# Performance work log

Hardware: AMD Instinct MI355X
Metric: run time of the kernel (lower is better)

The kernel has to match this reference:

```python
import jax, jax.numpy as jnp
import numpy as np

# MXInt config (mirrors q_config in init_kwargs)
A_MW, A_EW = 8, 4   # matmul input A mantissa/exponent widths
B_MW, B_EW = 8, 4   # matmul input B
O_MW, O_EW = 8, 4   # matmul output
SM_MW, SM_EW = 8, 4 # softmax output


def _dequant(m, e, mw):
    # m: [..., S, D] integer-valued mantissas; e: [..., S] shared row exponent
    # value = m * 2^(e - mw + 1)
    return m * jnp.exp2(e.astype(m.dtype)[..., None] - (mw - 1))


def _quant(x, mw, ew):
    # MXInt block quantization with exponent shared over the last dim.
    amax = jnp.max(jnp.abs(x), axis=-1)
    e = jnp.floor(jnp.log2(jnp.maximum(amax, jnp.exp2(jnp.float32(-126)))))
    e = jnp.clip(e, -(2 ** (ew - 1)), 2 ** (ew - 1) - 1)
    m = jnp.round(x * jnp.exp2(-(e[..., None] - (mw - 1))))
    m = jnp.clip(m, -(2 ** (mw - 1)), 2 ** (mw - 1) - 1)
    return m, e


def setup_inputs() -> dict:
    key = jax.random.key(0)
    ks = jax.random.split(key, 6)
    B, S, D = 256, 512, 64
    mquery = jax.random.randint(ks[0], (B, S, D), 0, 128).astype(jnp.float32)
    mkey = jax.random.randint(ks[1], (B, S, D), 0, 128).astype(jnp.float32)
    mvalue = jax.random.randint(ks[2], (B, S, D), 0, 128).astype(jnp.float32)
    equery = jax.random.randint(ks[3], (B, S), 0, 6, dtype=jnp.int32)
    ekey = jax.random.randint(ks[4], (B, S), 0, 6, dtype=jnp.int32)
    evalue = jax.random.randint(ks[5], (B, S), 0, 6, dtype=jnp.int32)
    return {"mquery": mquery, "equery": equery, "mkey": mkey,
            "ekey": ekey, "mvalue": mvalue, "evalue": evalue}


def reference(mquery, equery, mkey, ekey, mvalue, evalue):
    # QK^T in dequantized domain, then requantize output to MXInt (per-row exp)
    q = _dequant(mquery, equery, A_MW)            # [B,S,D]
    k = _dequant(mkey, ekey, B_MW)                # [B,S,D]
    scores = jnp.einsum('bsd,btd->bst', q, k)     # [B,S,S]
    m_s, _e_s = _quant(scores, O_MW, O_EW)
    # Note: the torch module calls the softmax on the score MANTISSAS only
    # (the score exponent is dropped), then requantizes the probabilities.
    probs = jax.nn.softmax(m_s, axis=-1)
    m_p, e_p = _quant(probs, SM_MW, SM_EW)
    # AV matmul: dequant probs with A widths, values with B widths
    p = _dequant(m_p, e_p, A_MW)                  # [B,S,S]
    v = _dequant(mvalue, evalue, B_MW)            # [B,S,D]
    ctx = jnp.einsum('bst,btd->bsd', p, v)        # [B,S,D]
    m_c, e_c = _quant(ctx, O_MW, O_EW)
    # final dequant exactly as the module: m * 2^(e - OUT_MAN_WIDTH + 1)
    return m_c * jnp.exp2(e_c[..., None] - O_MW + 1)
```

## Files before the change

### kernel.cpp

```cpp
#include <hip/hip_runtime.h>
#include <math.h>

#define S_LEN 512
#define D_DIM 64

typedef __attribute__((ext_vector_type(8))) short bf16x8;
typedef __attribute__((ext_vector_type(4))) float f32x4;
typedef __attribute__((ext_vector_type(4))) unsigned int u32x4;
typedef unsigned int u32;
typedef unsigned long long u64;

__device__ __forceinline__ float pow2i(int e) {
    return __int_as_float((e + 127) << 23);
}
__device__ __forceinline__ u32 pack_bf2(float lo, float hi) {
    return __builtin_amdgcn_perm(__float_as_uint(hi), __float_as_uint(lo), 0x07060302u);
}

extern "C" __global__ void __launch_bounds__(512, 2)
mxattn(const float* __restrict__ gmq, const int* __restrict__ geq,
       const float* __restrict__ gmk, const int* __restrict__ gek,
       const float* __restrict__ gmv, const int* __restrict__ gev,
       float* __restrict__ gout)
{
    __shared__ __attribute__((aligned(16))) short Ktile[32768];
    __shared__ __attribute__((aligned(16))) short Vtile[32768];
    __shared__ __attribute__((aligned(16))) char Pex[8 * 2 * 64 * 16];
    __shared__ __attribute__((aligned(16))) float evtab[S_LEN];

    const int b    = blockIdx.x;
    const int tid  = threadIdx.x;
    const int lane = tid & 63;
    const int wave = tid >> 6;
    const int l15  = lane & 15;
    const int lg   = lane >> 4;

    const float* mqb = gmq + (size_t)b * (S_LEN * D_DIM);
    const float* mkb = gmk + (size_t)b * (S_LEN * D_DIM);
    const float* mvb = gmv + (size_t)b * (S_LEN * D_DIM);
    const int* eqb = geq + b * S_LEN;
    const int* ekb = gek + b * S_LEN;
    const int* evb = gev + b * S_LEN;

    char* kb = (char*)Ktile;
    char* vb = (char*)Vtile;

    evtab[tid] = pow2i(evb[tid] - 7);
    #pragma unroll
    for (int i = 0; i < 4; ++i) {
        int tt = wave * 4 + i;
        int t = tt * 16 + l15;
        float ks = pow2i(ekb[t] - 7);
        const float* kp = mkb + t * 64 + lg * 8;
        f32x4 a0 = *(const f32x4*)(kp);
        f32x4 a1 = *(const f32x4*)(kp + 4);
        f32x4 a2 = *(const f32x4*)(kp + 32);
        f32x4 a3 = *(const f32x4*)(kp + 36);
        u32x4 w0 = { pack_bf2(a0[0] * ks, a0[1] * ks), pack_bf2(a0[2] * ks, a0[3] * ks),
                     pack_bf2(a1[0] * ks, a1[1] * ks), pack_bf2(a1[2] * ks, a1[3] * ks) };
        u32x4 w1 = { pack_bf2(a2[0] * ks, a2[1] * ks), pack_bf2(a2[2] * ks, a2[3] * ks),
                     pack_bf2(a3[0] * ks, a3[1] * ks), pack_bf2(a3[2] * ks, a3[3] * ks) };
        *(u32x4*)(kb + tt * 2048 + lane * 16) = w0;
        *(u32x4*)(kb + tt * 2048 + 1024 + lane * 16) = w1;
    }
    __syncthreads();

    #pragma unroll
    for (int i = 0; i < 8; ++i) {
        int idx = wave * 8 + i;
        int tb = (idx >> 2) * 32 + lg * 8;
        int dcol = (idx & 3) * 16 + l15;
        float v0 = mvb[(tb + 0) * 64 + dcol] * evtab[tb + 0];
        float v1 = mvb[(tb + 1) * 64 + dcol] * evtab[tb + 1];
        float v2 = mvb[(tb + 2) * 64 + dcol] * evtab[tb + 2];
        float v3 = mvb[(tb + 3) * 64 + dcol] * evtab[tb + 3];
        float v4 = mvb[(tb + 4) * 64 + dcol] * evtab[tb + 4];
        float v5 = mvb[(tb + 5) * 64 + dcol] * evtab[tb + 5];
        float v6 = mvb[(tb + 6) * 64 + dcol] * evtab[tb + 6];
        float v7 = mvb[(tb + 7) * 64 + dcol] * evtab[tb + 7];
        u32x4 wv = { pack_bf2(v0, v1), pack_bf2(v2, v3),
                     pack_bf2(v4, v5), pack_bf2(v6, v7) };
        *(u32x4*)(vb + idx * 1024 + lane * 16) = wv;
    }
    float sqp[4];
    #pragma unroll
    for (int p = 0; p < 4; ++p) sqp[p] = pow2i(eqb[p * 128 + wave * 16 + l15] - 7);
    __syncthreads();

    const float L2E = 1.44269504088896340736f;
    const int p_ = lg >> 1;
    const int srcA = l15 + ((lg & 1) << 5);
    const int srcAoff = srcA * 16 + (p_ << 3);

    for (int pass = 0; pass < 4; ++pass) {
        const int r0 = pass * 128 + wave * 16;

        bf16x8 qa0, qa1;
        {
            const float* qp = mqb + (size_t)(r0 + l15) * 64 + lg * 8;
            f32x4 a0 = *(const f32x4*)(qp);
            f32x4 a1 = *(const f32x4*)(qp + 4);
            f32x4 a2 = *(const f32x4*)(qp + 32);
            f32x4 a3 = *(const f32x4*)(qp + 36);
            u32x4 q0 = { pack_bf2(a0[0], a0[1]), pack_bf2(a0[2], a0[3]),
                         pack_bf2(a1[0], a1[1]), pack_bf2(a1[2], a1[3]) };
            u32x4 q1 = { pack_bf2(a2[0], a2[1]), pack_bf2(a2[2], a2[3]),
                         pack_bf2(a3[0], a3[1]), pack_bf2(a3[2], a3[3]) };
            qa0 = *(bf16x8*)&q0;
            qa1 = *(bf16x8*)&q1;
        }

        f32x4 acc[32];
        #pragma unroll
        for (int tt = 0; tt < 32; ++tt) acc[tt] = f32x4{0.f, 0.f, 0.f, 0.f};
        #pragma unroll
        for (int tt = 0; tt < 32; ++tt) {
            bf16x8 kf0 = *(const bf16x8*)(kb + tt * 2048 + lane * 16);
            bf16x8 kf1 = *(const bf16x8*)(kb + tt * 2048 + 1024 + lane * 16);
            acc[tt] = __builtin_amdgcn_mfma_f32_16x16x32_bf16(kf0, qa0, acc[tt], 0, 0, 0);
            acc[tt] = __builtin_amdgcn_mfma_f32_16x16x32_bf16(kf1, qa1, acc[tt], 0, 0, 0);
        }

        float am0 = 0.f, am1 = 0.f, am2 = 0.f, am3 = 0.f;
        #pragma unroll
        for (int tt = 0; tt < 32; ++tt) {
            am0 = fmaxf(am0, acc[tt][0]); am1 = fmaxf(am1, acc[tt][1]);
            am2 = fmaxf(am2, acc[tt][2]); am3 = fmaxf(am3, acc[tt][3]);
        }
        float amax = fmaxf(fmaxf(am0, am1), fmaxf(am2, am3));
        amax = fmaxf(amax, __shfl_xor(amax, 16));
        amax = fmaxf(amax, __shfl_xor(amax, 32));

        const float sq = sqp[pass];
        float as = fmaxf(amax * sq, 1.17549435e-38f);
        int es = (int)((__float_as_uint(as) >> 23) & 0xFFu) - 127;
        es = es < -8 ? -8 : (es > 7 ? 7 : es);
        const float c1 = sq * pow2i(7 - es);
        const float M = fminf(rintf(amax * c1), 127.f);
        const float nML2E = -M * L2E;

        float s0 = 0.f, s1 = 0.f, s2 = 0.f, s3 = 0.f;
        #pragma unroll
        for (int tt = 0; tt < 32; ++tt) {
            f32x4 a = acc[tt];
            float m0 = fminf(rintf(a[0] * c1), 127.f);
            float m1 = fminf(rintf(a[1] * c1), 127.f);
            float m2 = fminf(rintf(a[2] * c1), 127.f);
            float m3 = fminf(rintf(a[3] * c1), 127.f);
            a[0] = exp2f(fmaf(m0, L2E, nML2E));
            a[1] = exp2f(fmaf(m1, L2E, nML2E));
            a[2] = exp2f(fmaf(m2, L2E, nML2E));
            a[3] = exp2f(fmaf(m3, L2E, nML2E));
            s0 += a[0]; s1 += a[1]; s2 += a[2]; s3 += a[3];
            acc[tt] = a;
        }
        float sum = (s0 + s1) + (s2 + s3);
        sum += __shfl_xor(sum, 16);
        sum += __shfl_xor(sum, 32);

        float pm = fmaxf(1.0f / sum, 1.17549435e-38f);
        int ep = (int)((__float_as_uint(pm) >> 23) & 0xFFu) - 127;
        ep = ep < -8 ? -8 : (ep > 7 ? 7 : ep);
        const float sp = pow2i(7 - ep) / sum;
        const float osc = pow2i(ep - 7);

        f32x4 ctx[4];
        #pragma unroll
        for (int dt = 0; dt < 4; ++dt) ctx[dt] = f32x4{0.f, 0.f, 0.f, 0.f};
        #pragma unroll
        for (int c = 0; c < 16; ++c) {
            char* pb = Pex + (size_t)(wave * 2 + (c & 1)) * 1024;
            f32x4 aA = acc[2 * c], aB = acc[2 * c + 1];
            float m0 = fminf(rintf(aA[0] * sp), 127.f);
            float m1 = fminf(rintf(aA[1] * sp), 127.f);
            float m2 = fminf(rintf(aA[2] * sp), 127.f);
            float m3 = fminf(rintf(aA[3] * sp), 127.f);
            float m4 = fminf(rintf(aB[0] * sp), 127.f);
            float m5 = fminf(rintf(aB[1] * sp), 127.f);
            float m6 = fminf(rintf(aB[2] * sp), 127.f);
            float m7 = fminf(rintf(aB[3] * sp), 127.f);
            u32x4 wv = { pack_bf2(m0, m1), pack_bf2(m2, m3),
                         pack_bf2(m4, m5), pack_bf2(m6, m7) };
            *(u32x4*)(pb + lane * 16) = wv;
            asm volatile("s_waitcnt lgkmcnt(0)" ::: "memory");
            u64 pa = *(const u64*)(pb + srcAoff);
            u64 pc = *(const u64*)(pb + srcAoff + 256);
            union { u64 q[2]; bf16x8 h; } pu;
            pu.q[0] = pa; pu.q[1] = pc;
            bf16x8 pf = pu.h;
            #pragma unroll
            for (int dt = 0; dt < 4; ++dt) {
                bf16x8 vf = *(const bf16x8*)(vb + (c * 4 + dt) * 1024 + lane * 16);
                ctx[dt] = __builtin_amdgcn_mfma_f32_16x16x32_bf16(pf, vf, ctx[dt], 0, 0, 0);
            }
        }

        float oscr[4];
        #pragma unroll
        for (int j = 0; j < 4; ++j) oscr[j] = __shfl(osc, lg * 4 + j);
        float cv[4][4];
        float a4[4] = {0.f, 0.f, 0.f, 0.f};
        #pragma unroll
        for (int dt = 0; dt < 4; ++dt)
            #pragma unroll
            for (int j = 0; j < 4; ++j) {
                float x = ctx[dt][j] * oscr[j];
                cv[dt][j] = x;
                a4[j] = fmaxf(a4[j], fabsf(x));
            }
        #pragma unroll
        for (int j = 0; j < 4; ++j) {
            #pragma unroll
            for (int off = 1; off < 16; off <<= 1)
                a4[j] = fmaxf(a4[j], __shfl_xor(a4[j], off));
        }
        float csc[4], oo[4];
        #pragma unroll
        for (int j = 0; j < 4; ++j) {
            float a = fmaxf(a4[j], 1.17549435e-38f);
            int ec = (int)((__float_as_uint(a) >> 23) & 0xFFu) - 127;
            ec = ec < -8 ? -8 : (ec > 7 ? 7 : ec);
            csc[j] = pow2i(7 - ec);
            oo[j] = pow2i(ec - 7);
        }
        #pragma unroll
        for (int dt = 0; dt < 4; ++dt)
            #pragma unroll
            for (int j = 0; j < 4; ++j) {
                float m = rintf(cv[dt][j] * csc[j]);
                m = fminf(fmaxf(m, -128.f), 127.f);
                gout[((size_t)b * S_LEN + r0 + lg * 4 + j) * D_DIM + dt * 16 + l15] = m * oo[j];
            }
    }
}

extern "C" void kernel_launch(void* const* d_in, const int* in_sizes, int n_in,
                              void* d_out, int out_size, void* d_ws, size_t ws_size,
                              hipStream_t stream) {
    const float* mq = (const float*)d_in[0];
    const int*   eq = (const int*)d_in[1];
    const float* mk = (const float*)d_in[2];
    const int*   ek = (const int*)d_in[3];
    const float* mv = (const float*)d_in[4];
    const int*   ev = (const int*)d_in[5];
    float* out = (float*)d_out;
    int B = in_sizes[1] / S_LEN;
    mxattn<<<B, 512, 0, stream>>>(mq, eq, mk, ek, mv, ev, out);
}
```

Baseline: 65.03 us.

## Stage V tiles in global workspace to free LDS and double occupancy

Adds a new kernel variant that writes the bf16-converted, exponent-scaled V tile to a per-batch global workspace instead of LDS. LDS per block drops to roughly K tile plus a small exchange buffer, and launch bounds rise from 2 to 4 blocks per CU. V fragments are then read from global (L2-resident) memory with one-step prefetch inside the PV loop. The old LDS kernel stays as a fallback when the workspace is too small. The trade-off is higher-latency V reads and extra global write traffic in exchange for more concurrent blocks.

```diff
diff --git a/kernel.cpp b/kernel.cpp
--- a/kernel.cpp
+++ b/kernel.cpp
@@ -17,11 +17,259 @@
     return __builtin_amdgcn_perm(__float_as_uint(hi), __float_as_uint(lo), 0x07060302u);
 }
 
+extern "C" __global__ void __launch_bounds__(512, 4)
+mxattn_ws(const float* __restrict__ gmq, const int* __restrict__ geq,
+          const float* __restrict__ gmk, const int* __restrict__ gek,
+          const float* __restrict__ gmv, const int* __restrict__ gev,
+          float* __restrict__ gout, char* __restrict__ ws)
+{
+    __shared__ __attribute__((aligned(16))) short Ktile[32768];
+    __shared__ __attribute__((aligned(16))) char Pex[8 * 1024];
+    __shared__ __attribute__((aligned(16))) float evtab[S_LEN];
+
+    const int b    = blockIdx.x;
+    const int tid  = threadIdx.x;
+    const int lane = tid & 63;
+    const int wave = tid >> 6;
+    const int l15  = lane & 15;
+    const int lg   = lane >> 4;
+
+    const float* mqb = gmq + (size_t)b * (S_LEN * D_DIM);
+    const float* mkb = gmk + (size_t)b * (S_LEN * D_DIM);
+    const float* mvb = gmv + (size_t)b * (S_LEN * D_DIM);
+    const int* eqb = geq + b * S_LEN;
+    const int* ekb = gek + b * S_LEN;
+    const int* evb = gev + b * S_LEN;
+
+    char* kb  = (char*)Ktile;
+    char* vwb = ws + (size_t)b * 65536;
+
+    evtab[tid] = pow2i(evb[tid] - 7);
+    #pragma unroll
+    for (int i = 0; i < 4; ++i) {
+        int tt = wave * 4 + i;
+        int t = tt * 16 + l15;
+        float ks = pow2i(ekb[t] - 7);
+        const float* kp = mkb + t * 64 + lg * 8;
+        f32x4 a0 = *(const f32x4*)(kp);
+        f32x4 a1 = *(const f32x4*)(kp + 4);
+        f32x4 a2 = *(const f32x4*)(kp + 32);
+        f32x4 a3 = *(const f32x4*)(kp + 36);
+        u32x4 w0 = { pack_bf2(a0[0] * ks, a0[1] * ks), pack_bf2(a0[2] * ks, a0[3] * ks),
+                     pack_bf2(a1[0] * ks, a1[1] * ks), pack_bf2(a1[2] * ks, a1[3] * ks) };
+        u32x4 w1 = { pack_bf2(a2[0] * ks, a2[1] * ks), pack_bf2(a2[2] * ks, a2[3] * ks),
+                     pack_bf2(a3[0] * ks, a3[1] * ks), pack_bf2(a3[2] * ks, a3[3] * ks) };
+        *(u32x4*)(kb + tt * 2048 + lane * 16) = w0;
+        *(u32x4*)(kb + tt * 2048 + 1024 + lane * 16) = w1;
+    }
+    __syncthreads();
+
+    #pragma unroll
+    for (int i = 0; i < 8; ++i) {
+        int idx = wave * 8 + i;
+        int tb = (idx >> 2) * 32 + lg * 8;
+        int dcol = (idx & 3) * 16 + l15;
+        float v0 = mvb[(tb + 0) * 64 + dcol] * evtab[tb + 0];
+        float v1 = mvb[(tb + 1) * 64 + dcol] * evtab[tb + 1];
+        float v2 = mvb[(tb + 2) * 64 + dcol] * evtab[tb + 2];
+        float v3 = mvb[(tb + 3) * 64 + dcol] * evtab[tb + 3];
+        float v4 = mvb[(tb + 4) * 64 + dcol] * evtab[tb + 4];
+        float v5 = mvb[(tb + 5) * 64 + dcol] * evtab[tb + 5];
+        float v6 = mvb[(tb + 6) * 64 + dcol] * evtab[tb + 6];
+        float v7 = mvb[(tb + 7) * 64 + dcol] * evtab[tb + 7];
+        u32x4 wv = { pack_bf2(v0, v1), pack_bf2(v2, v3),
+                     pack_bf2(v4, v5), pack_bf2(v6, v7) };
+        *(u32x4*)(vwb + idx * 1024 + lane * 16) = wv;
+    }
+    float sqp[4];
+    #pragma unroll
+    for (int p = 0; p < 4; ++p) sqp[p] = pow2i(eqb[p * 128 + wave * 16 + l15] - 7);
+    __syncthreads();
+
+    const float L2E = 1.44269504088896340736f;
+    const int p_ = lg >> 1;
+    const int srcA = l15 + ((lg & 1) << 5);
+    const int srcAoff = srcA * 16 + (p_ << 3);
+    char* pb = Pex + wave * 1024;
+
+    for (int pass = 0; pass < 4; ++pass) {
+        const int r0 = pass * 128 + wave * 16;
+
+        bf16x8 qa0, qa1;
+        {
+            const float* qp = mqb + (size_t)(r0 + l15) * 64 + lg * 8;
+            f32x4 a0 = *(const f32x4*)(qp);
+            f32x4 a1 = *(const f32x4*)(qp + 4);
+            f32x4 a2 = *(const f32x4*)(qp + 32);
+            f32x4 a3 = *(const f32x4*)(qp + 36);
+            u32x4 q0 = { pack_bf2(a0[0], a0[1]), pack_bf2(a0[2], a0[3]),
+                         pack_bf2(a1[0], a1[1]), pack_bf2(a1[2], a1[3]) };
+            u32x4 q1 = { pack_bf2(a2[0], a2[1]), pack_bf2(a2[2], a2[3]),
+                         pack_bf2(a3[0], a3[1]), pack_bf2(a3[2], a3[3]) };
+            qa0 = *(bf16x8*)&q0;
+            qa1 = *(bf16x8*)&q1;
+        }
+
+        float amax = 0.f;
+        #pragma unroll
+        for (int h = 0; h < 2; ++h) {
+            f32x4 a[16];
+            #pragma unroll
+            for (int tt = 0; tt < 16; ++tt) a[tt] = f32x4{0.f, 0.f, 0.f, 0.f};
+            #pragma unroll
+            for (int tt = 0; tt < 16; ++tt) {
+                char* tp = kb + (h * 16 + tt) * 2048 + lane * 16;
+                bf16x8 kf0 = *(const bf16x8*)(tp);
+                bf16x8 kf1 = *(const bf16x8*)(tp + 1024);
+                a[tt] = __builtin_amdgcn_mfma_f32_16x16x32_bf16(kf0, qa0, a[tt], 0, 0, 0);
+                a[tt] = __builtin_amdgcn_mfma_f32_16x16x32_bf16(kf1, qa1, a[tt], 0, 0, 0);
+            }
+            #pragma unroll
+            for (int tt = 0; tt < 16; ++tt) {
+                amax = fmaxf(amax, fmaxf(fmaxf(a[tt][0], a[tt][1]),
+                                         fmaxf(a[tt][2], a[tt][3])));
+            }
+        }
+        amax = fmaxf(amax, __shfl_xor(amax, 16));
+        amax = fmaxf(amax, __shfl_xor(amax, 32));
+
+        const float sq = sqp[pass];
+        float as = fmaxf(amax * sq, 1.17549435e-38f);
+        int es = (int)((__float_as_uint(as) >> 23) & 0xFFu) - 127;
+        es = es < -8 ? -8 : (es > 7 ? 7 : es);
+        const float c1 = sq * pow2i(7 - es);
+        const float M = fminf(rintf(amax * c1), 127.f);
+        const float nML2E = -M * L2E;
+
+        u32 q8[32];
+        float sum = 0.f;
+        #pragma unroll
+        for (int h = 0; h < 2; ++h) {
+            f32x4 a[16];
+            #pragma unroll
+            for (int tt = 0; tt < 16; ++tt) a[tt] = f32x4{0.f, 0.f, 0.f, 0.f};
+            #pragma unroll
+            for (int tt = 0; tt < 16; ++tt) {
+                char* tp = kb + (h * 16 + tt) * 2048 + lane * 16;
+                bf16x8 kf0 = *(const bf16x8*)(tp);
+                bf16x8 kf1 = *(const bf16x8*)(tp + 1024);
+                a[tt] = __builtin_amdgcn_mfma_f32_16x16x32_bf16(kf0, qa0, a[tt], 0, 0, 0);
+                a[tt] = __builtin_amdgcn_mfma_f32_16x16x32_bf16(kf1, qa1, a[tt], 0, 0, 0);
+            }
+            #pragma unroll
+            for (int tt = 0; tt < 16; ++tt) {
+                float m0 = fminf(rintf(a[tt][0] * c1), 127.f);
+                float m1 = fminf(rintf(a[tt][1] * c1), 127.f);
+                float m2 = fminf(rintf(a[tt][2] * c1), 127.f);
+                float m3 = fminf(rintf(a[tt][3] * c1), 127.f);
+                sum += exp2f(fmaf(m0, L2E, nML2E));
+                sum += exp2f(fmaf(m1, L2E, nML2E));
+                sum += exp2f(fmaf(m2, L2E, nML2E));
+                sum += exp2f(fmaf(m3, L2E, nML2E));
+                q8[h * 16 + tt] = (u32)m0 | ((u32)m1 << 8) | ((u32)m2 << 16) | ((u32)m3 << 24);
+            }
+        }
+        sum += __shfl_xor(sum, 16);
+        sum += __shfl_xor(sum, 32);
+
+        float pm = fmaxf(1.0f / sum, 1.17549435e-38f);
+        int ep = (int)((__float_as_uint(pm) >> 23) & 0xFFu) - 127;
+        ep = ep < -8 ? -8 : (ep > 7 ? 7 : ep);
+        const float sp = pow2i(7 - ep) / sum;
+        const float osc = pow2i(ep - 7);
+
+        f32x4 ctx[4];
+        #pragma unroll
+        for (int dt = 0; dt < 4; ++dt) ctx[dt] = f32x4{0.f, 0.f, 0.f, 0.f};
+        bf16x8 vn0 = *(const bf16x8*)(vwb + 0 * 1024 + lane * 16);
+        bf16x8 vn1 = *(const bf16x8*)(vwb + 1 * 1024 + lane * 16);
+        bf16x8 vn2 = *(const bf16x8*)(vwb + 2 * 1024 + lane * 16);
+        bf16x8 vn3 = *(const bf16x8*)(vwb + 3 * 1024 + lane * 16);
+        #pragma unroll
+        for (int c = 0; c < 16; ++c) {
+            bf16x8 vc0 = vn0, vc1 = vn1, vc2 = vn2, vc3 = vn3;
+            u32 qlo = q8[2 * c], qhi = q8[2 * c + 1];
+            float e0 = exp2f(fmaf((float)(qlo & 0xFFu),         L2E, nML2E));
+            float e1 = exp2f(fmaf((float)((qlo >> 8) & 0xFFu),  L2E, nML2E));
+            float e2 = exp2f(fmaf((float)((qlo >> 16) & 0xFFu), L2E, nML2E));
+            float e3 = exp2f(fmaf((float)(qlo >> 24),           L2E, nML2E));
+            float e4 = exp2f(fmaf((float)(qhi & 0xFFu),         L2E, nML2E));
+            float e5 = exp2f(fmaf((float)((qhi >> 8) & 0xFFu),  L2E, nML2E));
+            float e6 = exp2f(fmaf((float)((qhi >> 16) & 0xFFu), L2E, nML2E));
+            float e7 = exp2f(fmaf((float)(qhi >> 24),           L2E, nML2E));
+            float m0 = fminf(rintf(e0 * sp), 127.f);
+            float m1 = fminf(rintf(e1 * sp), 127.f);
+            float m2 = fminf(rintf(e2 * sp), 127.f);
+            float m3 = fminf(rintf(e3 * sp), 127.f);
+            float m4 = fminf(rintf(e4 * sp), 127.f);
+            float m5 = fminf(rintf(e5 * sp), 127.f);
+            float m6 = fminf(rintf(e6 * sp), 127.f);
+            float m7 = fminf(rintf(e7 * sp), 127.f);
+            u32x4 wv = { pack_bf2(m0, m1), pack_bf2(m2, m3),
+                         pack_bf2(m4, m5), pack_bf2(m6, m7) };
+            *(u32x4*)(pb + lane * 16) = wv;
+            asm volatile("s_waitcnt lgkmcnt(0)" ::: "memory");
+            if (c < 15) {
+                vn0 = *(const bf16x8*)(vwb + ((c + 1) * 4 + 0) * 1024 + lane * 16);
+                vn1 = *(const bf16x8*)(vwb + ((c + 1) * 4 + 1) * 1024 + lane * 16);
+                vn2 = *(const bf16x8*)(vwb + ((c + 1) * 4 + 2) * 1024 + lane * 16);
+                vn3 = *(const bf16x8*)(vwb + ((c + 1) * 4 + 3) * 1024 + lane * 16);
+            }
+            u64 pa = *(const u64*)(pb + srcAoff);
+            u64 pc = *(const u64*)(pb + srcAoff + 256);
+            union { u64 q[2]; bf16x8 h; } pu;
+            pu.q[0] = pa; pu.q[1] = pc;
+            bf16x8 pf = pu.h;
+            ctx[0] = __builtin_amdgcn_mfma_f32_16x16x32_bf16(pf, vc0, ctx[0], 0, 0, 0);
+            ctx[1] = __builtin_amdgcn_mfma_f32_16x16x32_bf16(pf, vc1, ctx[1], 0, 0, 0);
+            ctx[2] = __builtin_amdgcn_mfma_f32_16x16x32_bf16(pf, vc2, ctx[2], 0, 0, 0);
+            ctx[3] = __builtin_amdgcn_mfma_f32_16x16x32_bf16(pf, vc3, ctx[3], 0, 0, 0);
+        }
+
+        float oscr[4];
+        #pragma unroll
+        for (int j = 0; j < 4; ++j) oscr[j] = __shfl(osc, lg * 4 + j);
+        float cv[4][4];
+        float a4[4] = {0.f, 0.f, 0.f, 0.f};
+        #pragma unroll
+        for (int dt = 0; dt < 4; ++dt)
+            #pragma unroll
+            for (int j = 0; j < 4; ++j) {
+                float x = ctx[dt][j] * oscr[j];
+                cv[dt][j] = x;
+                a4[j] = fmaxf(a4[j], fabsf(x));
+            }
+        #pragma unroll
+        for (int j = 0; j < 4; ++j) {
+            #pragma unroll
+            for (int off = 1; off < 16; off <<= 1)
+                a4[j] = fmaxf(a4[j], __shfl_xor(a4[j], off));
+        }
+        float csc[4], oo[4];
+        #pragma unroll
+        for (int j = 0; j < 4; ++j) {
+            float a = fmaxf(a4[j], 1.17549435e-38f);
+            int ec = (int)((__float_as_uint(a) >> 23) & 0xFFu) - 127;
+            ec = ec < -8 ? -8 : (ec > 7 ? 7 : ec);
+            csc[j] = pow2i(7 - ec);
+            oo[j] = pow2i(ec - 7);
+        }
+        #pragma unroll
+        for (int dt = 0; dt < 4; ++dt)
+            #pragma unroll
+            for (int j = 0; j < 4; ++j) {
+                float m = rintf(cv[dt][j] * csc[j]);
+                m = fminf(fmaxf(m, -128.f), 127.f);
+                gout[((size_t)b * S_LEN + r0 + lg * 4 + j) * D_DIM + dt * 16 + l15] = m * oo[j];
+            }
+    }
+}
+
 extern "C" __global__ void __launch_bounds__(512, 2)
-mxattn(const float* __restrict__ gmq, const int* __restrict__ geq,
-       const float* __restrict__ gmk, const int* __restrict__ gek,
-       const float* __restrict__ gmv, const int* __restrict__ gev,
-       float* __restrict__ gout)
+mxattn_lds(const float* __restrict__ gmq, const int* __restrict__ geq,
+           const float* __restrict__ gmk, const int* __restrict__ gek,
+           const float* __restrict__ gmv, const int* __restrict__ gev,
+           float* __restrict__ gout)
 {
     __shared__ __attribute__((aligned(16))) short Ktile[32768];
     __shared__ __attribute__((aligned(16))) short Vtile[32768];
@@ -245,5 +493,10 @@
     const int*   ev = (const int*)d_in[5];
     float* out = (float*)d_out;
     int B = in_sizes[1] / S_LEN;
-    mxattn<<<B, 512, 0, stream>>>(mq, eq, mk, ek, mv, ev, out);
+    size_t need = (size_t)B * 65536;
+    if (ws_size >= need && d_ws != nullptr) {
+        mxattn_ws<<<B, 512, 0, stream>>>(mq, eq, mk, ek, mv, ev, out, (char*)d_ws);
+    } else {
+        mxattn_lds<<<B, 512, 0, stream>>>(mq, eq, mk, ek, mv, ev, out);
+    }
 }
```

Result: slower. 208.3 us (+220.2%).

## Split each row tile's key range across wave pairs with 1024-thread blocks

Applied to the files above, without the earlier changes.

Doubles the block to 16 waves and has each pair of waves split the 512 keys of a 16-row tile in half. Partial row max, softmax sum and the PV context are exchanged through shared memory with block-wide barriers. Each wave then stores half of the output columns. The aim is to halve per-wave register pressure (16 accumulator tiles instead of 32) and put more waves on each CU to hide latency, at the cost of six block-wide syncs per pass and more LDS traffic.

```diff
diff --git a/kernel.cpp b/kernel.cpp
--- a/kernel.cpp
+++ b/kernel.cpp
@@ -17,7 +17,7 @@
     return __builtin_amdgcn_perm(__float_as_uint(hi), __float_as_uint(lo), 0x07060302u);
 }
 
-extern "C" __global__ void __launch_bounds__(512, 2)
+extern "C" __global__ void __launch_bounds__(1024, 4)
 mxattn(const float* __restrict__ gmq, const int* __restrict__ geq,
        const float* __restrict__ gmk, const int* __restrict__ gek,
        const float* __restrict__ gmv, const int* __restrict__ gev,
@@ -25,13 +25,15 @@
 {
     __shared__ __attribute__((aligned(16))) short Ktile[32768];
     __shared__ __attribute__((aligned(16))) short Vtile[32768];
-    __shared__ __attribute__((aligned(16))) char Pex[8 * 2 * 64 * 16];
-    __shared__ __attribute__((aligned(16))) float evtab[S_LEN];
+    __shared__ __attribute__((aligned(16))) char Pex[16 * 1024];
+    __shared__ __attribute__((aligned(16))) char Comb[16 * 1024];
 
     const int b    = blockIdx.x;
     const int tid  = threadIdx.x;
     const int lane = tid & 63;
     const int wave = tid >> 6;
+    const int grp  = wave >> 1;
+    const int h    = wave & 1;
     const int l15  = lane & 15;
     const int lg   = lane >> 4;
 
@@ -45,10 +47,11 @@
     char* kb = (char*)Ktile;
     char* vb = (char*)Vtile;
 
-    evtab[tid] = pow2i(evb[tid] - 7);
+    float* evt = (float*)Comb;
+    if (tid < S_LEN) evt[tid] = pow2i(evb[tid] - 7);
     #pragma unroll
-    for (int i = 0; i < 4; ++i) {
-        int tt = wave * 4 + i;
+    for (int i = 0; i < 2; ++i) {
+        int tt = wave * 2 + i;
         int t = tt * 16 + l15;
         float ks = pow2i(ekb[t] - 7);
         const float* kp = mkb + t * 64 + lg * 8;
@@ -66,34 +69,39 @@
     __syncthreads();
 
     #pragma unroll
-    for (int i = 0; i < 8; ++i) {
-        int idx = wave * 8 + i;
+    for (int i = 0; i < 4; ++i) {
+        int idx = wave * 4 + i;
         int tb = (idx >> 2) * 32 + lg * 8;
         int dcol = (idx & 3) * 16 + l15;
-        float v0 = mvb[(tb + 0) * 64 + dcol] * evtab[tb + 0];
-        float v1 = mvb[(tb + 1) * 64 + dcol] * evtab[tb + 1];
-        float v2 = mvb[(tb + 2) * 64 + dcol] * evtab[tb + 2];
-        float v3 = mvb[(tb + 3) * 64 + dcol] * evtab[tb + 3];
-        float v4 = mvb[(tb + 4) * 64 + dcol] * evtab[tb + 4];
-        float v5 = mvb[(tb + 5) * 64 + dcol] * evtab[tb + 5];
-        float v6 = mvb[(tb + 6) * 64 + dcol] * evtab[tb + 6];
-        float v7 = mvb[(tb + 7) * 64 + dcol] * evtab[tb + 7];
+        float v0 = mvb[(tb + 0) * 64 + dcol] * evt[tb + 0];
+        float v1 = mvb[(tb + 1) * 64 + dcol] * evt[tb + 1];
+        float v2 = mvb[(tb + 2) * 64 + dcol] * evt[tb + 2];
+        float v3 = mvb[(tb + 3) * 64 + dcol] * evt[tb + 3];
+        float v4 = mvb[(tb + 4) * 64 + dcol] * evt[tb + 4];
+        float v5 = mvb[(tb + 5) * 64 + dcol] * evt[tb + 5];
+        float v6 = mvb[(tb + 6) * 64 + dcol] * evt[tb + 6];
+        float v7 = mvb[(tb + 7) * 64 + dcol] * evt[tb + 7];
         u32x4 wv = { pack_bf2(v0, v1), pack_bf2(v2, v3),
                      pack_bf2(v4, v5), pack_bf2(v6, v7) };
         *(u32x4*)(vb + idx * 1024 + lane * 16) = wv;
     }
     float sqp[4];
     #pragma unroll
-    for (int p = 0; p < 4; ++p) sqp[p] = pow2i(eqb[p * 128 + wave * 16 + l15] - 7);
+    for (int p = 0; p < 4; ++p) sqp[p] = pow2i(eqb[p * 128 + grp * 16 + l15] - 7);
     __syncthreads();
 
     const float L2E = 1.44269504088896340736f;
     const int p_ = lg >> 1;
     const int srcA = l15 + ((lg & 1) << 5);
     const int srcAoff = srcA * 16 + (p_ << 3);
+    char* pb = Pex + wave * 1024;
+    char* cb_self = Comb + wave * 1024 + lane * 16;
+    char* cb_peer = Comb + (wave ^ 1) * 1024 + lane * 16;
+    char* px_self = Pex + wave * 1024 + lane * 16;
+    char* px_peer = Pex + (wave ^ 1) * 1024 + lane * 16;
 
     for (int pass = 0; pass < 4; ++pass) {
-        const int r0 = pass * 128 + wave * 16;
+        const int r0 = pass * 128 + grp * 16;
 
         bf16x8 qa0, qa1;
         {
@@ -110,26 +118,30 @@
             qa1 = *(bf16x8*)&q1;
         }
 
-        f32x4 acc[32];
-        #pragma unroll
-        for (int tt = 0; tt < 32; ++tt) acc[tt] = f32x4{0.f, 0.f, 0.f, 0.f};
-        #pragma unroll
-        for (int tt = 0; tt < 32; ++tt) {
-            bf16x8 kf0 = *(const bf16x8*)(kb + tt * 2048 + lane * 16);
-            bf16x8 kf1 = *(const bf16x8*)(kb + tt * 2048 + 1024 + lane * 16);
-            acc[tt] = __builtin_amdgcn_mfma_f32_16x16x32_bf16(kf0, qa0, acc[tt], 0, 0, 0);
-            acc[tt] = __builtin_amdgcn_mfma_f32_16x16x32_bf16(kf1, qa1, acc[tt], 0, 0, 0);
+        f32x4 acc[16];
+        #pragma unroll
+        for (int lt = 0; lt < 16; ++lt) acc[lt] = f32x4{0.f, 0.f, 0.f, 0.f};
+        #pragma unroll
+        for (int lt = 0; lt < 16; ++lt) {
+            char* tp = kb + (h * 16 + lt) * 2048 + lane * 16;
+            bf16x8 kf0 = *(const bf16x8*)(tp);
+            bf16x8 kf1 = *(const bf16x8*)(tp + 1024);
+            acc[lt] = __builtin_amdgcn_mfma_f32_16x16x32_bf16(kf0, qa0, acc[lt], 0, 0, 0);
+            acc[lt] = __builtin_amdgcn_mfma_f32_16x16x32_bf16(kf1, qa1, acc[lt], 0, 0, 0);
         }
 
         float am0 = 0.f, am1 = 0.f, am2 = 0.f, am3 = 0.f;
         #pragma unroll
-        for (int tt = 0; tt < 32; ++tt) {
-            am0 = fmaxf(am0, acc[tt][0]); am1 = fmaxf(am1, acc[tt][1]);
-            am2 = fmaxf(am2, acc[tt][2]); am3 = fmaxf(am3, acc[tt][3]);
+        for (int lt = 0; lt < 16; ++lt) {
+            am0 = fmaxf(am0, acc[lt][0]); am1 = fmaxf(am1, acc[lt][1]);
+            am2 = fmaxf(am2, acc[lt][2]); am3 = fmaxf(am3, acc[lt][3]);
         }
         float amax = fmaxf(fmaxf(am0, am1), fmaxf(am2, am3));
         amax = fmaxf(amax, __shfl_xor(amax, 16));
         amax = fmaxf(amax, __shfl_xor(amax, 32));
+        *(float*)cb_self = amax;
+        __syncthreads();
+        amax = fmaxf(amax, *(const float*)cb_peer);
 
         const float sq = sqp[pass];
         float as = fmaxf(amax * sq, 1.17549435e-38f);
@@ -141,8 +153,8 @@
 
         float s0 = 0.f, s1 = 0.f, s2 = 0.f, s3 = 0.f;
         #pragma unroll
-        for (int tt = 0; tt < 32; ++tt) {
-            f32x4 a = acc[tt];
+        for (int lt = 0; lt < 16; ++lt) {
+            f32x4 a = acc[lt];
             float m0 = fminf(rintf(a[0] * c1), 127.f);
             float m1 = fminf(rintf(a[1] * c1), 127.f);
             float m2 = fminf(rintf(a[2] * c1), 127.f);
@@ -152,11 +164,14 @@
             a[2] = exp2f(fmaf(m2, L2E, nML2E));
             a[3] = exp2f(fmaf(m3, L2E, nML2E));
             s0 += a[0]; s1 += a[1]; s2 += a[2]; s3 += a[3];
-            acc[tt] = a;
+            acc[lt] = a;
         }
         float sum = (s0 + s1) + (s2 + s3);
         sum += __shfl_xor(sum, 16);
         sum += __shfl_xor(sum, 32);
+        *(float*)(cb_self + 4) = sum;
+        __syncthreads();
+        sum += *(const float*)(cb_peer + 4);
 
         float pm = fmaxf(1.0f / sum, 1.17549435e-38f);
         int ep = (int)((__float_as_uint(pm) >> 23) & 0xFFu) - 127;
@@ -168,8 +183,8 @@
         #pragma unroll
         for (int dt = 0; dt < 4; ++dt) ctx[dt] = f32x4{0.f, 0.f, 0.f, 0.f};
         #pragma unroll
-        for (int c = 0; c < 16; ++c) {
-            char* pb = Pex + (size_t)(wave * 2 + (c & 1)) * 1024;
+        for (int c = 0; c < 8; ++c) {
+            int C = h * 8 + c;
             f32x4 aA = acc[2 * c], aB = acc[2 * c + 1];
             float m0 = fminf(rintf(aA[0] * sp), 127.f);
             float m1 = fminf(rintf(aA[1] * sp), 127.f);
@@ -185,15 +200,28 @@
             asm volatile("s_waitcnt lgkmcnt(0)" ::: "memory");
             u64 pa = *(const u64*)(pb + srcAoff);
             u64 pc = *(const u64*)(pb + srcAoff + 256);
-            union { u64 q[2]; bf16x8 h; } pu;
+            union { u64 q[2]; bf16x8 hh; } pu;
             pu.q[0] = pa; pu.q[1] = pc;
-            bf16x8 pf = pu.h;
+            bf16x8 pf = pu.hh;
             #pragma unroll
             for (int dt = 0; dt < 4; ++dt) {
-                bf16x8 vf = *(const bf16x8*)(vb + (c * 4 + dt) * 1024 + lane * 16);
+                bf16x8 vf = *(const bf16x8*)(vb + (C * 4 + dt) * 1024 + lane * 16);
                 ctx[dt] = __builtin_amdgcn_mfma_f32_16x16x32_bf16(pf, vf, ctx[dt], 0, 0, 0);
             }
         }
+
+        *(f32x4*)cb_self = ctx[0];
+        __syncthreads();
+        ctx[0] += *(const f32x4*)cb_peer;
+        *(f32x4*)px_self = ctx[1];
+        __syncthreads();
+        ctx[1] += *(const f32x4*)px_peer;
+        *(f32x4*)cb_self = ctx[2];
+        __syncthreads();
+        ctx[2] += *(const f32x4*)cb_peer;
+        *(f32x4*)px_self = ctx[3];
+        __syncthreads();
+        ctx[3] += *(const f32x4*)px_peer;
 
         float oscr[4];
         #pragma unroll
@@ -224,13 +252,15 @@
             oo[j] = pow2i(ec - 7);
         }
         #pragma unroll
-        for (int dt = 0; dt < 4; ++dt)
+        for (int i = 0; i < 2; ++i) {
+            int dt = 2 * h + i;
             #pragma unroll
             for (int j = 0; j < 4; ++j) {
                 float m = rintf(cv[dt][j] * csc[j]);
                 m = fminf(fmaxf(m, -128.f), 127.f);
                 gout[((size_t)b * S_LEN + r0 + lg * 4 + j) * D_DIM + dt * 16 + l15] = m * oo[j];
             }
+        }
     }
 }
 
@@ -245,5 +275,5 @@
     const int*   ev = (const int*)d_in[5];
     float* out = (float*)d_out;
     int B = in_sizes[1] / S_LEN;
-    mxattn<<<B, 512, 0, stream>>>(mq, eq, mk, ek, mv, ev, out);
-}
+    mxattn<<<B, 1024, 0, stream>>>(mq, eq, mk, ek, mv, ev, out);
+}
```

Result: slower. 78.12 us (+20.1%).
